# Performance work log

Measured on AMD Instinct MI355X. Metric: run time of the kernel, lower is better.

The kernel has to match this reference:

```python
import jax, jax.numpy as jnp
import numpy as np
import math

B, S, HID = 1, 2048, 1024
H = 16
D = HID // H          # head_dim = 64
M = 128               # RFF num_features
SIGMA = 1.0
ALPHA = 0.9
NORMALIZE = True


def setup_inputs() -> dict:
    key = jax.random.key(0)
    ks = jax.random.split(key, 12)
    s = 1.0 / math.sqrt(HID)  # nn.Linear default-ish init scale
    inp = {
        "hidden_states": jax.random.normal(ks[0], (B, S, HID), dtype=jnp.float32),
        "attention_mask": jnp.zeros((B, 1, 1, S), dtype=jnp.float32),  # 0 = attend
        "Wq": jax.random.uniform(ks[1], (HID, HID), minval=-s, maxval=s, dtype=jnp.float32),
        "bq": jnp.zeros((HID,), dtype=jnp.float32),
        "Wk": jax.random.uniform(ks[2], (HID, HID), minval=-s, maxval=s, dtype=jnp.float32),
        "bk": jnp.zeros((HID,), dtype=jnp.float32),
        "Wv": jax.random.uniform(ks[3], (HID, HID), minval=-s, maxval=s, dtype=jnp.float32),
        "bv": jnp.zeros((HID,), dtype=jnp.float32),
        "Wo": jax.random.uniform(ks[4], (HID, HID), minval=-s, maxval=s, dtype=jnp.float32),
        "bo": jnp.zeros((HID,), dtype=jnp.float32),
        # RFF kernel params per head: omega ~ N(0, 1/sigma^2), phase b ~ U[0, 2pi]
        "omega": jax.random.normal(ks[5], (H, D, M), dtype=jnp.float32) / SIGMA,
        "rff_b": jax.random.uniform(ks[6], (H, M), minval=0.0, maxval=2.0 * math.pi, dtype=jnp.float32),
    }
    return inp


def _heads(x):
    # (B, S, HID) -> (B, H, S, D)
    return x.reshape(B, S, H, D).transpose(0, 2, 1, 3)


def _phi(x, omega, rff_b):
    # x: (B, H, S, D) -> (B, H, S, M) random Fourier features
    proj = jnp.einsum("bhsd,hdm->bhsm", x, omega) + rff_b[None, :, None, :]
    phi = math.sqrt(2.0 / M) * jnp.cos(proj)
    if NORMALIZE:
        phi = phi / (jnp.linalg.norm(phi, axis=-1, keepdims=True) + 1e-6)
    return phi


def reference(hidden_states, attention_mask, Wq, bq, Wk, bk, Wv, bv, Wo, bo, omega, rff_b):
    q = _heads(hidden_states @ Wq.T + bq)   # (B,H,S,D)
    k = _heads(hidden_states @ Wk.T + bk)
    v = _heads(hidden_states @ Wv.T + bv)

    qn = q / (jnp.linalg.norm(q, axis=-1, keepdims=True) + 1e-6)
    kn = k / (jnp.linalg.norm(k, axis=-1, keepdims=True) + 1e-6)

    dot_scores = jnp.einsum("bhqd,bhkd->bhqk", q, k)             # standard QK^T
    kernel_scores = jnp.einsum("bhqm,bhkm->bhqk",
                               _phi(qn, omega, rff_b),
                               _phi(kn, omega, rff_b))            # phi(Q)phi(K)^T

    scores = (ALPHA * dot_scores + (1.0 - ALPHA) * kernel_scores) / math.sqrt(D)
    scores = scores + attention_mask * -10000.0
    weights = jax.nn.softmax(scores, axis=-1)                     # dropout: eval mode (identity)

    context = jnp.einsum("bhqk,bhkd->bhqd", weights, v)
    context = context.transpose(0, 2, 1, 3).reshape(B, S, HID)
    return context @ Wo.T + bo
```

## Files before the change

kernel.cpp:

```cpp
#include <hip/hip_runtime.h>
#include <math.h>

#define S_LEN 2048
#define HID   1024
#define NH    16
#define HD    64
#define NM    128
#define CAUG  192
#define KC    64
#define NT    (S_LEN / KC)

constexpr float ALPHA = 0.9f;

typedef __attribute__((ext_vector_type(8))) short bf16x8;
typedef __attribute__((ext_vector_type(4))) short bf16x4;
typedef __attribute__((ext_vector_type(4))) float f32x4;
typedef __attribute__((ext_vector_type(4))) int   int4v;

#define MFMA(a,b,c) __builtin_amdgcn_mfma_f32_16x16x32_bf16(a,b,c,0,0,0)

static __device__ inline short f2bf(float f) {
    unsigned u = __float_as_uint(f);
    u += 0x7fffu + ((u >> 16) & 1u);
    return (short)(u >> 16);
}
static __device__ inline float bf2f(short s) {
    return __uint_as_float(((unsigned)(unsigned short)s) << 16);
}

__global__ __launch_bounds__(256)
void conv_kernel(const float* __restrict__ hs,
                 const float* __restrict__ Wq, const float* __restrict__ Wk,
                 const float* __restrict__ Wv, const float* __restrict__ Wo,
                 const float* __restrict__ omega,
                 short* __restrict__ hsb, short* __restrict__ wqb, short* __restrict__ wkb,
                 short* __restrict__ wvb, short* __restrict__ wob, short* __restrict__ omtb)
{
    int i = blockIdx.x * 256 + threadIdx.x;
    if (i >= 1605632) return;
    if (i >= 1572864) {
        int j = (i - 1572864) * 4;
        int h = j >> 13, rem = j & 8191;
        int d = rem >> 7, m = rem & 127;
        float4 v = *(const float4*)(omega + j);
        short* dst = omtb + ((h * 128 + m) << 6) + d;
        dst[0]       = f2bf(v.x);
        dst[64]      = f2bf(v.y);
        dst[128]     = f2bf(v.z);
        dst[192]     = f2bf(v.w);
        return;
    }
    const float* src; short* dst; int off;
    if (i < 524288) { src = hs; dst = hsb; off = i; }
    else {
        int j = i - 524288;
        int r = j >> 18;
        off = j & 262143;
        src = (r == 0) ? Wq : (r == 1) ? Wk : (r == 2) ? Wv : Wo;
        dst = (r == 0) ? wqb : (r == 1) ? wkb : (r == 2) ? wvb : wob;
    }
    float4 v = ((const float4*)src)[off];
    bf16x4 o; o[0] = f2bf(v.x); o[1] = f2bf(v.y); o[2] = f2bf(v.z); o[3] = f2bf(v.w);
    ((bf16x4*)dst)[off] = o;
}

__global__ __launch_bounds__(256)
void gemm_mfma(const short* __restrict__ A,
               const short* __restrict__ W0, const float* __restrict__ b0, void* C0,
               const short* __restrict__ W1, const float* __restrict__ b1, void* C1,
               const short* __restrict__ W2, const float* __restrict__ b2, void* C2,
               int m0_, int m1_, int m2_, int Mrows)
{
    const short* W; const float* bias; void* C; int mode;
    if (blockIdx.z == 0)      { W = W0; bias = b0; C = C0; mode = m0_; }
    else if (blockIdx.z == 1) { W = W1; bias = b1; C = C1; mode = m1_; }
    else                      { W = W2; bias = b2; C = C2; mode = m2_; }

    __shared__ short As[128][40];
    __shared__ short Bs[128][40];

    const int tid = threadIdx.x;
    const int wave = tid >> 6, lane = tid & 63;
    const int l15 = lane & 15, l4 = lane >> 4;
    const int wm = wave >> 1, wn = wave & 1;
    const int m0 = blockIdx.y * 128, n0 = blockIdx.x * 128;

    const int srow = (tid >> 2);
    const int scol = (tid & 3) * 16;

    f32x4 acc[4][4];
#pragma unroll
    for (int i = 0; i < 4; ++i)
#pragma unroll
        for (int j = 0; j < 4; ++j) acc[i][j] = (f32x4){0.f,0.f,0.f,0.f};

    int4v apre[2], bpre[2];
#pragma unroll
    for (int it = 0; it < 2; ++it) {
        apre[it] = *(const int4v*)((const char*)A + (size_t)(m0 + srow + it*64) * 2048 + scol);
        bpre[it] = *(const int4v*)((const char*)W + (size_t)(n0 + srow + it*64) * 2048 + scol);
    }

    for (int ks = 0; ks < 32; ++ks) {
        __syncthreads();
#pragma unroll
        for (int it = 0; it < 2; ++it) {
            *(int4v*)((char*)&As[0][0] + (srow + it*64) * 80 + scol) = apre[it];
            *(int4v*)((char*)&Bs[0][0] + (srow + it*64) * 80 + scol) = bpre[it];
        }
        __syncthreads();
        if (ks + 1 < 32) {
            const int kb = (ks + 1) * 64;
#pragma unroll
            for (int it = 0; it < 2; ++it) {
                apre[it] = *(const int4v*)((const char*)A + (size_t)(m0 + srow + it*64) * 2048 + kb + scol);
                bpre[it] = *(const int4v*)((const char*)W + (size_t)(n0 + srow + it*64) * 2048 + kb + scol);
            }
        }
        bf16x8 af[4], bf[4];
#pragma unroll
        for (int mi = 0; mi < 4; ++mi)
            af[mi] = *(const bf16x8*)((const char*)&As[0][0] + (wm*64 + mi*16 + l15) * 80 + l4*16);
#pragma unroll
        for (int nj = 0; nj < 4; ++nj)
            bf[nj] = *(const bf16x8*)((const char*)&Bs[0][0] + (wn*64 + nj*16 + l15) * 80 + l4*16);
#pragma unroll
        for (int mi = 0; mi < 4; ++mi)
#pragma unroll
            for (int nj = 0; nj < 4; ++nj)
                acc[mi][nj] = MFMA(af[mi], bf[nj], acc[mi][nj]);
    }

#pragma unroll
    for (int nj = 0; nj < 4; ++nj) {
        const int nglob = n0 + wn*64 + nj*16 + l15;
        const float bn = bias[nglob];
#pragma unroll
        for (int mi = 0; mi < 4; ++mi) {
            const int mbase = m0 + wm*64 + mi*16 + l4*4;
            if (mode == 0) {
#pragma unroll
                for (int r = 0; r < 4; ++r)
                    ((short*)C)[(size_t)(mbase + r) * 1024 + nglob] = f2bf(acc[mi][nj][r] + bn);
            } else if (mode == 1) {
                bf16x4 pk;
#pragma unroll
                for (int r = 0; r < 4; ++r) pk[r] = f2bf(acc[mi][nj][r] + bn);
                *(bf16x4*)((short*)C + (size_t)nglob * Mrows + mbase) = pk;
            } else {
#pragma unroll
                for (int r = 0; r < 4; ++r)
                    ((float*)C)[(size_t)(mbase + r) * 1024 + nglob] = acc[mi][nj][r] + bn;
            }
        }
    }
}

__global__ __launch_bounds__(256)
void phi2_kernel(const short* __restrict__ qbuf, const short* __restrict__ kbuf,
                 const short* __restrict__ omtb, const float* __restrict__ rffb,
                 short* __restrict__ Qa, short* __restrict__ Ka)
{
    __shared__ short om[128][72];
    __shared__ float bsh[128];

    const int src = blockIdx.z, h = blockIdx.y;
    const int s0 = blockIdx.x * 64;
    const short* X = src ? kbuf : qbuf;
    short* Out     = src ? Ka : Qa;
    const float fq   = src ? 1.0f : (ALPHA * 0.125f);
    const float fphi = src ? 1.0f : ((1.0f - ALPHA) * 0.125f);

    const int tid = threadIdx.x, wave = tid >> 6, lane = tid & 63;
    const int l15 = lane & 15, l4 = lane >> 4;

    {
        const char* gsrc = (const char*)(omtb + ((size_t)h << 13));
#pragma unroll
        for (int it = 0; it < 4; ++it) {
            int f = tid * 16 + it * 4096;
            int row = f >> 7, colb = f & 127;
            *(int4v*)((char*)&om[0][0] + row * 144 + colb) = *(const int4v*)(gsrc + f);
        }
        if (tid < 128) bsh[tid] = rffb[h * 128 + tid];
    }
    __syncthreads();

    const int srow = s0 + wave * 16 + l15;

    bf16x8 xf[2];
#pragma unroll
    for (int cs = 0; cs < 2; ++cs)
        xf[cs] = *(const bf16x8*)(X + (size_t)srow * HID + h * HD + cs * 32 + l4 * 8);

    float ss = 0.f;
#pragma unroll
    for (int cs = 0; cs < 2; ++cs)
#pragma unroll
        for (int j = 0; j < 8; ++j) { float v = bf2f(xf[cs][j]); ss = fmaf(v, v, ss); }
    ss += __shfl_xor(ss, 16);
    ss += __shfl_xor(ss, 32);
    const float inv = 1.0f / (sqrtf(ss) + 1e-6f);

    bf16x8 qn[2];
#pragma unroll
    for (int cs = 0; cs < 2; ++cs) {
        bf16x8 o, w;
#pragma unroll
        for (int j = 0; j < 8; ++j) {
            float v = bf2f(xf[cs][j]);
            o[j] = f2bf(v * inv);
            w[j] = f2bf(v * fq);
        }
        qn[cs] = o;
        *(bf16x8*)(Out + ((size_t)h * S_LEN + srow) * CAUG + cs * 32 + l4 * 8) = w;
    }

    f32x4 pacc[8];
#pragma unroll
    for (int t = 0; t < 8; ++t) pacc[t] = (f32x4){0.f,0.f,0.f,0.f};
#pragma unroll
    for (int t = 0; t < 8; ++t)
#pragma unroll
        for (int cs = 0; cs < 2; ++cs) {
            bf16x8 bf = *(const bf16x8*)((const char*)&om[0][0] + (t*16 + l15) * 144 + cs*64 + l4*16);
            pacc[t] = MFMA(qn[cs], bf, pacc[t]);
        }

    float ph[8][4];
    float ps[4] = {0.f, 0.f, 0.f, 0.f};
#pragma unroll
    for (int t = 0; t < 8; ++t) {
        const float bv = bsh[t * 16 + l15];
#pragma unroll
        for (int r = 0; r < 4; ++r) {
            float p = pacc[t][r] + bv;
            float c = 0.125f * __cosf(p);
            ph[t][r] = c;
            ps[r] = fmaf(c, c, ps[r]);
        }
    }
#pragma unroll
    for (int r = 0; r < 4; ++r) {
        ps[r] += __shfl_xor(ps[r], 1);
        ps[r] += __shfl_xor(ps[r], 2);
        ps[r] += __shfl_xor(ps[r], 4);
        ps[r] += __shfl_xor(ps[r], 8);
    }
    float inv2[4];
#pragma unroll
    for (int r = 0; r < 4; ++r) inv2[r] = fphi / (sqrtf(ps[r]) + 1e-6f);

#pragma unroll
    for (int t = 0; t < 8; ++t)
#pragma unroll
        for (int r = 0; r < 4; ++r)
            Out[((size_t)h * S_LEN + s0 + wave * 16 + l4 * 4 + r) * CAUG + 64 + t * 16 + l15]
                = f2bf(ph[t][r] * inv2[r]);
}

__global__ __launch_bounds__(256)
void flash_mfma(const short* __restrict__ Qa, const short* __restrict__ Ka,
                const short* __restrict__ vt, const float* __restrict__ mask,
                short* __restrict__ ctxb)
{
    __shared__ short Ks[64][200];
    __shared__ short Vt[64][72];
    __shared__ short Pl[4][16][72];

    const int tid = threadIdx.x;
    const int wave = tid >> 6, lane = tid & 63;
    const int l15 = lane & 15, l4 = lane >> 4;
    const int h = blockIdx.y;
    const int q0 = blockIdx.x * 64 + wave * 16;

    bf16x8 qf[6];
#pragma unroll
    for (int cs = 0; cs < 6; ++cs)
        qf[cs] = *(const bf16x8*)(Qa + ((size_t)h * 2048 + q0 + l15) * CAUG + cs*32 + l4*8);

    f32x4 oacc[4];
#pragma unroll
    for (int di = 0; di < 4; ++di) oacc[di] = (f32x4){0.f,0.f,0.f,0.f};
    float mreg = -1e30f, lreg = 0.f;

    int kr[6], kcb[6], vr[2], vcb[2];
#pragma unroll
    for (int it = 0; it < 6; ++it) { int f = tid*16 + it*4096; kr[it] = f/384; kcb[it] = f%384; }
#pragma unroll
    for (int it = 0; it < 2; ++it) { int f = tid*16 + it*4096; vr[it] = f/128; vcb[it] = f%128; }

    const char* Kg = (const char*)(Ka + (size_t)h * 2048 * CAUG);
    const char* Vg = (const char*)(vt + (size_t)h * 64 * 2048);

    int4v kpre[6], vpre[2];
#pragma unroll
    for (int it = 0; it < 6; ++it) kpre[it] = *(const int4v*)(Kg + (size_t)kr[it]*384 + kcb[it]);
#pragma unroll
    for (int it = 0; it < 2; ++it) vpre[it] = *(const int4v*)(Vg + (size_t)vr[it]*4096 + vcb[it]);

    for (int kt = 0; kt < NT; ++kt) {
        __syncthreads();
#pragma unroll
        for (int it = 0; it < 6; ++it)
            *(int4v*)((char*)&Ks[0][0] + kr[it]*400 + kcb[it]) = kpre[it];
#pragma unroll
        for (int it = 0; it < 2; ++it)
            *(int4v*)((char*)&Vt[0][0] + vr[it]*144 + vcb[it]) = vpre[it];
        __syncthreads();
        if (kt + 1 < NT) {
            const size_t ko = (size_t)(kt + 1) * 64 * 384;
            const size_t vo = (size_t)(kt + 1) * 128;
#pragma unroll
            for (int it = 0; it < 6; ++it) kpre[it] = *(const int4v*)(Kg + ko + (size_t)kr[it]*384 + kcb[it]);
#pragma unroll
            for (int it = 0; it < 2; ++it) vpre[it] = *(const int4v*)(Vg + (size_t)vr[it]*4096 + vo + vcb[it]);
        }

        f32x4 sacc[4];
#pragma unroll
        for (int fi = 0; fi < 4; ++fi) sacc[fi] = (f32x4){0.f,0.f,0.f,0.f};
#pragma unroll
        for (int cs = 0; cs < 6; ++cs) {
            bf16x8 ka[4];
#pragma unroll
            for (int fi = 0; fi < 4; ++fi)
                ka[fi] = *(const bf16x8*)((const char*)&Ks[0][0] + (fi*16 + l15)*400 + cs*64 + l4*16);
#pragma unroll
            for (int fi = 0; fi < 4; ++fi)
                sacc[fi] = MFMA(ka[fi], qf[cs], sacc[fi]);
        }
#pragma unroll
        for (int fi = 0; fi < 4; ++fi) {
            float4 mk = *(const float4*)&mask[kt*64 + fi*16 + l4*4];
#pragma unroll
            for (int r = 0; r < 4; ++r)
                sacc[fi][r] += ((const float*)&mk)[r] * -10000.f;
        }
        {
            float pm = -1e30f;
#pragma unroll
            for (int fi = 0; fi < 4; ++fi)
#pragma unroll
                for (int r = 0; r < 4; ++r) pm = fmaxf(pm, sacc[fi][r]);
            pm = fmaxf(pm, __shfl_xor(pm, 16));
            pm = fmaxf(pm, __shfl_xor(pm, 32));
            const float mnew = fmaxf(mreg, pm);
            const float sc = __expf(mreg - mnew);
            mreg = mnew;
            float ps = 0.f;
#pragma unroll
            for (int fi = 0; fi < 4; ++fi)
#pragma unroll
                for (int r = 0; r < 4; ++r) {
                    float p = __expf(sacc[fi][r] - mnew);
                    sacc[fi][r] = p;
                    ps += p;
                }
            ps += __shfl_xor(ps, 16);
            ps += __shfl_xor(ps, 32);
            lreg = lreg * sc + ps;
#pragma unroll
            for (int di = 0; di < 4; ++di)
#pragma unroll
                for (int r = 0; r < 4; ++r) oacc[di][r] *= sc;
#pragma unroll
            for (int fi = 0; fi < 4; ++fi) {
                bf16x4 pk;
#pragma unroll
                for (int r = 0; r < 4; ++r) pk[r] = f2bf(sacc[fi][r]);
                *(bf16x4*)(&Pl[wave][l15][fi*16 + l4*4]) = pk;
            }
        }
#pragma unroll
        for (int cs2 = 0; cs2 < 2; ++cs2) {
            bf16x8 va[4], pb;
#pragma unroll
            for (int di = 0; di < 4; ++di)
                va[di] = *(const bf16x8*)((const char*)&Vt[0][0] + (di*16 + l15)*144 + cs2*64 + l4*16);
            pb = *(const bf16x8*)((const char*)&Pl[wave][0][0] + l15*144 + cs2*64 + l4*16);
#pragma unroll
            for (int di = 0; di < 4; ++di)
                oacc[di] = MFMA(va[di], pb, oacc[di]);
        }
    }

    {
        const float inv = 1.0f / lreg;
        const int s = q0 + l15;
#pragma unroll
        for (int di = 0; di < 4; ++di) {
            bf16x4 o;
#pragma unroll
            for (int r = 0; r < 4; ++r) o[r] = f2bf(oacc[di][r] * inv);
            *(bf16x4*)(ctxb + (size_t)s * HID + h*64 + di*16 + l4*4) = o;
        }
    }
}

extern "C" void kernel_launch(void* const* d_in, const int* in_sizes, int n_in,
                              void* d_out, int out_size, void* d_ws, size_t ws_size,
                              hipStream_t stream)
{
    const float* hs    = (const float*)d_in[0];
    const float* mask  = (const float*)d_in[1];
    const float* Wq    = (const float*)d_in[2];
    const float* bq    = (const float*)d_in[3];
    const float* Wk    = (const float*)d_in[4];
    const float* bk    = (const float*)d_in[5];
    const float* Wv    = (const float*)d_in[6];
    const float* bv    = (const float*)d_in[7];
    const float* Wo    = (const float*)d_in[8];
    const float* bo    = (const float*)d_in[9];
    const float* omega = (const float*)d_in[10];
    const float* rffb  = (const float*)d_in[11];
    float* out = (float*)d_out;

    short* wsS = (short*)d_ws;
    short* hsb = wsS;
    short* wqb = hsb + 2097152;
    short* wkb = wqb + 1048576;
    short* wvb = wkb + 1048576;
    short* wob = wvb + 1048576;
    short* qb  = wob + 1048576;
    short* kb  = qb  + 2097152;
    short* vtb = kb  + 2097152;
    short* ctxb= vtb + 2097152;
    short* QaB = ctxb+ 2097152;
    short* KaB = QaB + 6291456;
    short* omtb= KaB + 6291456;

    conv_kernel<<<6272, 256, 0, stream>>>(hs, Wq, Wk, Wv, Wo, omega,
                                          hsb, wqb, wkb, wvb, wob, omtb);
    gemm_mfma<<<dim3(8, 16, 3), 256, 0, stream>>>(hsb, wqb, bq, qb, wkb, bk, kb, wvb, bv, vtb,
                                                  0, 0, 1, S_LEN);
    phi2_kernel<<<dim3(32, 16, 2), 256, 0, stream>>>(qb, kb, omtb, rffb, QaB, KaB);
    flash_mfma<<<dim3(32, 16), 256, 0, stream>>>(QaB, KaB, vtb, mask, ctxb);
    gemm_mfma<<<dim3(8, 16, 1), 256, 0, stream>>>(ctxb, wob, bo, out, wob, bo, out, wob, bo, out,
                                                  2, 2, 2, S_LEN);
}
```

Measured before the change: 140.8 us.

## Split flash attention keys across wave groups and drop online softmax max

Restructures the attention kernel so two wave groups each process half of the key sequence in 32-key chunks, with each wave owning 32 query rows instead of 16. K fragments are therefore reused across two query tiles. The running-max and rescaling of online softmax is removed: exponentials are taken directly, relying on the scores staying bounded. The partial outputs and row sums of the two groups are combined through shared memory at the end. This cuts the per-tile softmax work and the serial loop length, at the risk of overflow if scores grow large and with more registers per thread (launch bounds set for 2 blocks per CU).

New measurement: 127.6 us. 1.1x faster.

```diff
diff --git a/kernel.cpp b/kernel.cpp
--- a/kernel.cpp
+++ b/kernel.cpp
@@ -7,8 +7,8 @@
 #define HD    64
 #define NM    128
 #define CAUG  192
-#define KC    64
-#define NT    (S_LEN / KC)
+#define KC2   32
+#define NCH   32
 
 constexpr float ALPHA = 0.9f;
 
@@ -259,141 +259,157 @@
                 = f2bf(ph[t][r] * inv2[r]);
 }
 
-__global__ __launch_bounds__(256)
+__global__ __launch_bounds__(256, 2)
 void flash_mfma(const short* __restrict__ Qa, const short* __restrict__ Ka,
                 const short* __restrict__ vt, const float* __restrict__ mask,
                 short* __restrict__ ctxb)
 {
-    __shared__ short Ks[64][200];
-    __shared__ short Vt[64][72];
-    __shared__ short Pl[4][16][72];
+    __shared__ short Ks[2][32][200];
+    __shared__ short Vt[2][64][40];
+    __shared__ short Pl[4][32][40];
 
     const int tid = threadIdx.x;
     const int wave = tid >> 6, lane = tid & 63;
     const int l15 = lane & 15, l4 = lane >> 4;
+    const int g = wave >> 1, sub = wave & 1;
     const int h = blockIdx.y;
-    const int q0 = blockIdx.x * 64 + wave * 16;
-
-    bf16x8 qf[6];
-#pragma unroll
-    for (int cs = 0; cs < 6; ++cs)
-        qf[cs] = *(const bf16x8*)(Qa + ((size_t)h * 2048 + q0 + l15) * CAUG + cs*32 + l4*8);
-
-    f32x4 oacc[4];
-#pragma unroll
-    for (int di = 0; di < 4; ++di) oacc[di] = (f32x4){0.f,0.f,0.f,0.f};
-    float mreg = -1e30f, lreg = 0.f;
-
+    const int q0 = blockIdx.x * 64 + sub * 32;
+
+    bf16x8 qf[2][6];
+#pragma unroll
+    for (int qj = 0; qj < 2; ++qj)
+#pragma unroll
+        for (int cs = 0; cs < 6; ++cs)
+            qf[qj][cs] = *(const bf16x8*)(Qa + ((size_t)h * 2048 + q0 + qj*16 + l15) * CAUG + cs*32 + l4*8);
+
+    f32x4 oacc[4][2];
+#pragma unroll
+    for (int di = 0; di < 4; ++di)
+#pragma unroll
+        for (int qj = 0; qj < 2; ++qj) oacc[di][qj] = (f32x4){0.f,0.f,0.f,0.f};
+    float lsum[2] = {0.f, 0.f};
+
+    const int t = tid & 127;
     int kr[6], kcb[6], vr[2], vcb[2];
 #pragma unroll
-    for (int it = 0; it < 6; ++it) { int f = tid*16 + it*4096; kr[it] = f/384; kcb[it] = f%384; }
-#pragma unroll
-    for (int it = 0; it < 2; ++it) { int f = tid*16 + it*4096; vr[it] = f/128; vcb[it] = f%128; }
+    for (int it = 0; it < 6; ++it) { int f = t*16 + it*2048; kr[it] = f/384; kcb[it] = f%384; }
+#pragma unroll
+    for (int it = 0; it < 2; ++it) { int f = t*16 + it*2048; vr[it] = f/64; vcb[it] = f%64; }
 
     const char* Kg = (const char*)(Ka + (size_t)h * 2048 * CAUG);
     const char* Vg = (const char*)(vt + (size_t)h * 64 * 2048);
 
     int4v kpre[6], vpre[2];
 #pragma unroll
-    for (int it = 0; it < 6; ++it) kpre[it] = *(const int4v*)(Kg + (size_t)kr[it]*384 + kcb[it]);
-#pragma unroll
-    for (int it = 0; it < 2; ++it) vpre[it] = *(const int4v*)(Vg + (size_t)vr[it]*4096 + vcb[it]);
-
-    for (int kt = 0; kt < NT; ++kt) {
+    for (int it = 0; it < 6; ++it)
+        kpre[it] = *(const int4v*)(Kg + (size_t)(g*NCH)*12288 + (size_t)kr[it]*384 + kcb[it]);
+#pragma unroll
+    for (int it = 0; it < 2; ++it)
+        vpre[it] = *(const int4v*)(Vg + (size_t)vr[it]*4096 + (size_t)(g*NCH)*64 + vcb[it]);
+
+    for (int i = 0; i < NCH; ++i) {
+        const int kt = g * NCH + i;
         __syncthreads();
 #pragma unroll
         for (int it = 0; it < 6; ++it)
-            *(int4v*)((char*)&Ks[0][0] + kr[it]*400 + kcb[it]) = kpre[it];
+            *(int4v*)((char*)&Ks[g][0][0] + kr[it]*400 + kcb[it]) = kpre[it];
 #pragma unroll
         for (int it = 0; it < 2; ++it)
-            *(int4v*)((char*)&Vt[0][0] + vr[it]*144 + vcb[it]) = vpre[it];
+            *(int4v*)((char*)&Vt[g][0][0] + vr[it]*80 + vcb[it]) = vpre[it];
         __syncthreads();
-        if (kt + 1 < NT) {
-            const size_t ko = (size_t)(kt + 1) * 64 * 384;
-            const size_t vo = (size_t)(kt + 1) * 128;
-#pragma unroll
-            for (int it = 0; it < 6; ++it) kpre[it] = *(const int4v*)(Kg + ko + (size_t)kr[it]*384 + kcb[it]);
-#pragma unroll
-            for (int it = 0; it < 2; ++it) vpre[it] = *(const int4v*)(Vg + (size_t)vr[it]*4096 + vo + vcb[it]);
-        }
-
-        f32x4 sacc[4];
-#pragma unroll
-        for (int fi = 0; fi < 4; ++fi) sacc[fi] = (f32x4){0.f,0.f,0.f,0.f};
+        if (i + 1 < NCH) {
+            const size_t ko = (size_t)(kt + 1) * 12288;
+            const size_t vo = (size_t)(kt + 1) * 64;
+#pragma unroll
+            for (int it = 0; it < 6; ++it)
+                kpre[it] = *(const int4v*)(Kg + ko + (size_t)kr[it]*384 + kcb[it]);
+#pragma unroll
+            for (int it = 0; it < 2; ++it)
+                vpre[it] = *(const int4v*)(Vg + (size_t)vr[it]*4096 + vo + vcb[it]);
+        }
+
+        f32x4 sacc[2][2];
+#pragma unroll
+        for (int fi = 0; fi < 2; ++fi)
+#pragma unroll
+            for (int qj = 0; qj < 2; ++qj) sacc[fi][qj] = (f32x4){0.f,0.f,0.f,0.f};
 #pragma unroll
         for (int cs = 0; cs < 6; ++cs) {
-            bf16x8 ka[4];
-#pragma unroll
-            for (int fi = 0; fi < 4; ++fi)
-                ka[fi] = *(const bf16x8*)((const char*)&Ks[0][0] + (fi*16 + l15)*400 + cs*64 + l4*16);
-#pragma unroll
-            for (int fi = 0; fi < 4; ++fi)
-                sacc[fi] = MFMA(ka[fi], qf[cs], sacc[fi]);
-        }
-#pragma unroll
-        for (int fi = 0; fi < 4; ++fi) {
-            float4 mk = *(const float4*)&mask[kt*64 + fi*16 + l4*4];
-#pragma unroll
-            for (int r = 0; r < 4; ++r)
-                sacc[fi][r] += ((const float*)&mk)[r] * -10000.f;
+            bf16x8 ka[2];
+#pragma unroll
+            for (int fi = 0; fi < 2; ++fi)
+                ka[fi] = *(const bf16x8*)((const char*)&Ks[g][0][0] + (fi*16 + l15)*400 + cs*64 + l4*16);
+#pragma unroll
+            for (int fi = 0; fi < 2; ++fi)
+#pragma unroll
+                for (int qj = 0; qj < 2; ++qj)
+                    sacc[fi][qj] = MFMA(ka[fi], qf[qj][cs], sacc[fi][qj]);
+        }
+#pragma unroll
+        for (int fi = 0; fi < 2; ++fi) {
+            float4 mk = *(const float4*)&mask[kt*32 + fi*16 + l4*4];
+            float mv[4] = {mk.x * -10000.f, mk.y * -10000.f, mk.z * -10000.f, mk.w * -10000.f};
+#pragma unroll
+            for (int qj = 0; qj < 2; ++qj) {
+                bf16x4 pk;
+#pragma unroll
+                for (int r = 0; r < 4; ++r) {
+                    float p = __expf(sacc[fi][qj][r] + mv[r]);
+                    lsum[qj] += p;
+                    pk[r] = f2bf(p);
+                }
+                *(bf16x4*)((char*)&Pl[wave][0][0] + (qj*16 + l15)*80 + fi*32 + l4*8) = pk;
+            }
         }
         {
-            float pm = -1e30f;
-#pragma unroll
-            for (int fi = 0; fi < 4; ++fi)
-#pragma unroll
-                for (int r = 0; r < 4; ++r) pm = fmaxf(pm, sacc[fi][r]);
-            pm = fmaxf(pm, __shfl_xor(pm, 16));
-            pm = fmaxf(pm, __shfl_xor(pm, 32));
-            const float mnew = fmaxf(mreg, pm);
-            const float sc = __expf(mreg - mnew);
-            mreg = mnew;
-            float ps = 0.f;
-#pragma unroll
-            for (int fi = 0; fi < 4; ++fi)
-#pragma unroll
-                for (int r = 0; r < 4; ++r) {
-                    float p = __expf(sacc[fi][r] - mnew);
-                    sacc[fi][r] = p;
-                    ps += p;
-                }
-            ps += __shfl_xor(ps, 16);
-            ps += __shfl_xor(ps, 32);
-            lreg = lreg * sc + ps;
+            bf16x8 va[4], pb[2];
 #pragma unroll
             for (int di = 0; di < 4; ++di)
-#pragma unroll
-                for (int r = 0; r < 4; ++r) oacc[di][r] *= sc;
-#pragma unroll
-            for (int fi = 0; fi < 4; ++fi) {
-                bf16x4 pk;
-#pragma unroll
-                for (int r = 0; r < 4; ++r) pk[r] = f2bf(sacc[fi][r]);
-                *(bf16x4*)(&Pl[wave][l15][fi*16 + l4*4]) = pk;
+                va[di] = *(const bf16x8*)((const char*)&Vt[g][0][0] + (di*16 + l15)*80 + l4*16);
+#pragma unroll
+            for (int qj = 0; qj < 2; ++qj)
+                pb[qj] = *(const bf16x8*)((const char*)&Pl[wave][0][0] + (qj*16 + l15)*80 + l4*16);
+#pragma unroll
+            for (int di = 0; di < 4; ++di)
+#pragma unroll
+                for (int qj = 0; qj < 2; ++qj)
+                    oacc[di][qj] = MFMA(va[di], pb[qj], oacc[di][qj]);
+        }
+    }
+
+#pragma unroll
+    for (int qj = 0; qj < 2; ++qj) {
+        lsum[qj] += __shfl_xor(lsum[qj], 16);
+        lsum[qj] += __shfl_xor(lsum[qj], 32);
+    }
+
+    __syncthreads();
+    float* scrO = (float*)&Ks[0][0][0];
+    float* scrL = (float*)&Vt[0][0][0];
+    if (g == 1) {
+#pragma unroll
+        for (int qj = 0; qj < 2; ++qj) {
+#pragma unroll
+            for (int di = 0; di < 4; ++di)
+                *(f32x4*)&scrO[(size_t)(sub*32 + qj*16 + l15)*68 + di*16 + l4*4] = oacc[di][qj];
+            if (l4 == 0) scrL[sub*32 + qj*16 + l15] = lsum[qj];
+        }
+    }
+    __syncthreads();
+    if (g == 0) {
+#pragma unroll
+        for (int qj = 0; qj < 2; ++qj) {
+            const float l = lsum[qj] + scrL[sub*32 + qj*16 + l15];
+            const float inv = 1.0f / l;
+            const int s = q0 + qj*16 + l15;
+#pragma unroll
+            for (int di = 0; di < 4; ++di) {
+                f32x4 o2 = *(const f32x4*)&scrO[(size_t)(sub*32 + qj*16 + l15)*68 + di*16 + l4*4];
+                bf16x4 ob;
+#pragma unroll
+                for (int r = 0; r < 4; ++r) ob[r] = f2bf((oacc[di][qj][r] + o2[r]) * inv);
+                *(bf16x4*)(ctxb + (size_t)s * HID + h*64 + di*16 + l4*4) = ob;
             }
-        }
-#pragma unroll
-        for (int cs2 = 0; cs2 < 2; ++cs2) {
-            bf16x8 va[4], pb;
-#pragma unroll
-            for (int di = 0; di < 4; ++di)
-                va[di] = *(const bf16x8*)((const char*)&Vt[0][0] + (di*16 + l15)*144 + cs2*64 + l4*16);
-            pb = *(const bf16x8*)((const char*)&Pl[wave][0][0] + l15*144 + cs2*64 + l4*16);
-#pragma unroll
-            for (int di = 0; di < 4; ++di)
-                oacc[di] = MFMA(va[di], pb, oacc[di]);
-        }
-    }
-
-    {
-        const float inv = 1.0f / lreg;
-        const int s = q0 + l15;
-#pragma unroll
-        for (int di = 0; di < 4; ++di) {
-            bf16x4 o;
-#pragma unroll
-            for (int r = 0; r < 4; ++r) o[r] = f2bf(oacc[di][r] * inv);
-            *(bf16x4*)(ctxb + (size_t)s * HID + h*64 + di*16 + l4*4) = o;
         }
     }
 }
```
